# Optimization experiments

Measured on AMD Instinct MI355X. Metric: run time of the kernel, lower is better.

The kernel has to match this reference:

```python
import jax, jax.numpy as jnp
import numpy as np

E, CAP, D, H = 8, 2048, 1024, 4096  # experts, capacity, model_dim, hidden

def setup_inputs() -> dict:
    key = jax.random.key(0)
    k = jax.random.split(key, 5)
    s1 = 1.0 / np.sqrt(D)
    s2 = 1.0 / np.sqrt(H)
    return {
        "x": jax.random.normal(k[0], (E, CAP, D), dtype=jnp.float32),
        "fc1_w": jax.random.uniform(k[1], (E, H, D), jnp.float32, -s1, s1),
        "fc1_b": jax.random.uniform(k[2], (E, H), jnp.float32, -s1, s1),
        "fc2_w": jax.random.uniform(k[3], (E, H, D), jnp.float32, -s2, s2),
        "fc2_b": jax.random.uniform(k[4], (E, D), jnp.float32, -s2, s2),
    }

def reference(x, fc1_w, fc1_b, fc2_w, fc2_b):
    # y = relu(x @ fc1_w^T + b1) @ fc2_w + b2, batched over experts e
    y = jnp.einsum('ecd,ehd->ech', x, fc1_w) + fc1_b[:, None, :]   # [E, CAP, H]
    y = jax.nn.relu(y)
    y = jnp.einsum('ech,ehd->ecd', y, fc2_w) + fc2_b[:, None, :]   # [E, CAP, D]
    return y
```

## Files before the change

kernel.cpp:

```cpp
#include <hip/hip_runtime.h>
#include <hip/hip_bf16.h>
#include <stdint.h>

#define E_    8
#define CAP_  2048
#define D_    1024
#define H_    4096

typedef unsigned short u16;
typedef __attribute__((ext_vector_type(8))) short bf16x8;
typedef __attribute__((ext_vector_type(4))) float f32x4;

__device__ __forceinline__ u16 f2bf(float f) {
    union { float f; unsigned int u; } v; v.f = f;
    unsigned int u = v.u;
    unsigned int r = (u + 0x7fffu + ((u >> 16) & 1u)) >> 16;
    return (u16)r;
}

__device__ __forceinline__ void gload_lds16(const void* g, void* l) {
    __builtin_amdgcn_global_load_lds(
        (const __attribute__((address_space(1))) unsigned int*)g,
        (__attribute__((address_space(3))) unsigned int*)l,
        16, 0, 0);
}

__global__ void cvt_f32_bf16(const float* __restrict__ in, u16* __restrict__ out, int n4) {
    int i = blockIdx.x * blockDim.x + threadIdx.x;
    if (i >= n4) return;
    const float4 v = ((const float4*)in)[i];
    ushort4 o;
    o.x = f2bf(v.x); o.y = f2bf(v.y); o.z = f2bf(v.z); o.w = f2bf(v.w);
    ((ushort4*)out)[i] = o;
}

__global__ void transpose_cvt(const float* __restrict__ in, u16* __restrict__ out) {
    __shared__ float t[64][69];
    const int e  = blockIdx.z;
    const int h0 = blockIdx.y * 64;
    const int d0 = blockIdx.x * 64;
    const float* I = in + (size_t)e * H_ * D_;
    u16* O = out + (size_t)e * D_ * H_;
    const int tid = threadIdx.x;
    const int r  = tid >> 4;
    const int c  = (tid & 15) * 4;
    #pragma unroll
    for (int s = 0; s < 4; ++s) {
        const int h = r + s * 16;
        const float4 v = *(const float4*)&I[(size_t)(h0 + h) * D_ + d0 + c];
        t[h][c] = v.x; t[h][c + 1] = v.y; t[h][c + 2] = v.z; t[h][c + 3] = v.w;
    }
    __syncthreads();
    #pragma unroll
    for (int s = 0; s < 4; ++s) {
        const int d = r + s * 16;
        ushort4 o;
        o.x = f2bf(t[c + 0][d]); o.y = f2bf(t[c + 1][d]);
        o.z = f2bf(t[c + 2][d]); o.w = f2bf(t[c + 3][d]);
        *(ushort4*)&O[(size_t)(d0 + d) * H_ + h0 + c] = o;
    }
}

template<int EPI>
__global__ __launch_bounds__(512, 2) void gemm256(
    const u16* __restrict__ A, const u16* __restrict__ B,
    const float* __restrict__ bias, void* __restrict__ Cv,
    int M, int N, int K, int TM, int TN,
    size_t sA, size_t sB, size_t sBias, size_t sC)
{
    __shared__ __align__(16) u16 lds[2][2][2][128 * 64];

    const int nwg = gridDim.x;
    const int cpx = nwg >> 3;
    const int bid = blockIdx.x;
    const int wg  = (bid & 7) * cpx + (bid >> 3);
    const int tpe = TM * TN;
    const int e   = wg / tpe;
    const int rem = wg - e * tpe;
    const int tn  = rem / TM;
    const int tm  = rem - tn * TM;
    const int row0 = tm << 8;
    const int col0 = tn << 8;

    const u16* Ae = A + (size_t)e * sA;
    const u16* Be = B + (size_t)e * sB;

    const int tid  = threadIdx.x;
    const int lane = tid & 63;
    const int w    = tid >> 6;
    const int wr   = w >> 2;
    const int wc   = w & 3;
    const int wcH  = wc >> 1;
    const int wcL  = wc & 1;
    const int fr   = lane & 15;
    const int fq   = lane >> 4;
    const int cx   = (fq ^ (fr & 7)) << 4;
    const int lo0  = fr * 128 + cx;
    const int lo1  = fr * 128 + (cx ^ 64);
    const int sl   = lane ^ ((lane >> 3) & 7);
    const int NT   = K >> 6;

    const int srow = (w << 4) + (sl >> 3);
    const int scol = (sl & 7) << 3;
    const u16* pA[2][2];
    const u16* pB[2][2];
    #pragma unroll
    for (int l = 0; l < 2; ++l)
        #pragma unroll
        for (int hf = 0; hf < 2; ++hf) {
            pA[l][hf] = Ae + (size_t)(row0 + hf * 128 + srow + l * 8) * K + scol;
            pB[l][hf] = Be + (size_t)(col0 + hf * 128 + srow + l * 8) * K + scol;
        }

    auto stageA = [&](int buf, int hf, bool pred) {
        #pragma unroll
        for (int l = 0; l < 2; ++l) {
            if (pred) gload_lds16(pA[l][hf], &lds[buf][0][hf][(w * 2 + l) * 512]);
            pA[l][hf] += 64;
        }
    };
    auto stageB = [&](int buf, int hf, bool pred) {
        #pragma unroll
        for (int l = 0; l < 2; ++l) {
            if (pred) gload_lds16(pB[l][hf], &lds[buf][1][hf][(w * 2 + l) * 512]);
            pB[l][hf] += 64;
        }
    };

    f32x4 acc[8][4] = {};

    stageB(0, 0, true); stageB(0, 1, true);
    stageA(0, 0, true); stageA(0, 1, true);
    stageB(1, 0, true); stageB(1, 1, true);
    asm volatile("s_waitcnt vmcnt(4)");
    __builtin_amdgcn_s_barrier();

    for (int t = 0; t < NT; ++t) {
        const int db = t & 1;
        const char* Ah = (const char*)&lds[db][0][wr][0];
        const char* Bh = (const char*)&lds[db][1][wcH][0];
        bf16x8 b[4][2];
        #pragma unroll
        for (int n = 0; n < 4; ++n) {
            b[n][0] = *(const bf16x8*)(Bh + wcL * 8192 + n * 2048 + lo0);
            b[n][1] = *(const bf16x8*)(Bh + wcL * 8192 + n * 2048 + lo1);
        }
        #pragma unroll
        for (int p = 0; p < 4; ++p) {
            bf16x8 a[2][2];
            #pragma unroll
            for (int mm = 0; mm < 2; ++mm) {
                a[mm][0] = *(const bf16x8*)(Ah + (2 * p + mm) * 2048 + lo0);
                a[mm][1] = *(const bf16x8*)(Ah + (2 * p + mm) * 2048 + lo1);
            }
            if (p == 0)      stageA(db ^ 1, 0, t + 1 < NT);
            else if (p == 1) stageA(db ^ 1, 1, t + 1 < NT);
            else if (p == 2) stageB(db,     0, t + 2 < NT);
            else             stageB(db,     1, t + 2 < NT);

            __builtin_amdgcn_s_setprio(1);
            #pragma unroll
            for (int kk = 0; kk < 2; ++kk)
                #pragma unroll
                for (int mm = 0; mm < 2; ++mm)
                    #pragma unroll
                    for (int n = 0; n < 4; ++n)
                        acc[2 * p + mm][n] = __builtin_amdgcn_mfma_f32_16x16x32_bf16(
                            a[mm][kk], b[n][kk], acc[2 * p + mm][n], 0, 0, 0);
            __builtin_amdgcn_s_setprio(0);
            if (p == 3) {
                if (t < NT - 2)       asm volatile("s_waitcnt vmcnt(4)");
                else if (t == NT - 2) asm volatile("s_waitcnt vmcnt(0)");
            }
            __builtin_amdgcn_s_barrier();
        }
    }

    const float* be = bias + (size_t)e * sBias;
    if (EPI == 0) {
        u16* cl = (u16*)&lds[0][0][0][0];
        #pragma unroll
        for (int n = 0; n < 4; ++n) {
            const int ccol = wc * 64 + n * 16 + fr;
            const float bv = be[col0 + ccol];
            #pragma unroll
            for (int m = 0; m < 8; ++m) {
                const int crow = wr * 128 + m * 16 + fq * 4;
                #pragma unroll
                for (int i = 0; i < 4; ++i) {
                    float v = acc[m][n][i] + bv;
                    v = v > 0.f ? v : 0.f;
                    cl[(crow + i) * 256 + ccol] = f2bf(v);
                }
            }
        }
        __builtin_amdgcn_s_barrier();
        u16* Ce = (u16*)Cv + (size_t)e * sC;
        const int rr = tid >> 5;
        const int cc = (tid & 31) * 8;
        #pragma unroll
        for (int s = 0; s < 16; ++s) {
            const int row = s * 16 + rr;
            const float4 v = *(const float4*)&cl[row * 256 + cc];
            *(float4*)&Ce[(size_t)(row0 + row) * N + col0 + cc] = v;
        }
    } else {
        float* cf = (float*)&lds[0][0][0][0];
        float* Ce = (float*)Cv + (size_t)e * sC;
        #pragma unroll
        for (int p = 0; p < 2; ++p) {
            __builtin_amdgcn_s_barrier();
            #pragma unroll
            for (int n = 0; n < 4; ++n) {
                const int ccol = wc * 64 + n * 16 + fr;
                const float bv = be[col0 + ccol];
                #pragma unroll
                for (int mm = 0; mm < 4; ++mm) {
                    const int lrow = wr * 64 + mm * 16 + fq * 4;
                    #pragma unroll
                    for (int i = 0; i < 4; ++i)
                        cf[(lrow + i) * 256 + ccol] = acc[p * 4 + mm][n][i] + bv;
                }
            }
            __builtin_amdgcn_s_barrier();
            const int lr = tid >> 6;
            const int cc = (tid & 63) * 4;
            #pragma unroll
            for (int s = 0; s < 16; ++s) {
                const int lrow = s * 8 + lr;
                const int wrr  = lrow >> 6;
                const int rem2 = lrow & 63;
                const int grow = row0 + wrr * 128 + p * 64 + rem2;
                const float4 v = *(const float4*)&cf[lrow * 256 + cc];
                *(float4*)&Ce[(size_t)grow * N + col0 + cc] = v;
            }
        }
    }
}

extern "C" void kernel_launch(void* const* d_in, const int* in_sizes, int n_in,
                              void* d_out, int out_size, void* d_ws, size_t ws_size,
                              hipStream_t stream) {
    (void)in_sizes; (void)n_in; (void)out_size; (void)ws_size;
    const float* x     = (const float*)d_in[0];
    const float* fc1_w = (const float*)d_in[1];
    const float* fc1_b = (const float*)d_in[2];
    const float* fc2_w = (const float*)d_in[3];
    const float* fc2_b = (const float*)d_in[4];
    float* out = (float*)d_out;

    u16* xbf  = (u16*)d_ws;
    u16* w1bf = xbf  + (size_t)E_ * CAP_ * D_;
    u16* w2t  = w1bf + (size_t)E_ * H_ * D_;
    u16* y1   = w2t  + (size_t)E_ * D_ * H_;

    {
        int n4 = E_ * CAP_ * D_ / 4;
        cvt_f32_bf16<<<n4 / 256, 256, 0, stream>>>(x, xbf, n4);
    }
    {
        int n4 = E_ * H_ * D_ / 4;
        cvt_f32_bf16<<<n4 / 256, 256, 0, stream>>>(fc1_w, w1bf, n4);
    }
    transpose_cvt<<<dim3(D_ / 64, H_ / 64, E_), 256, 0, stream>>>(fc2_w, w2t);

    gemm256<0><<<dim3(E_ * (CAP_ / 256) * (H_ / 256)), 512, 0, stream>>>(
        xbf, w1bf, fc1_b, y1, CAP_, H_, D_, CAP_ / 256, H_ / 256,
        (size_t)CAP_ * D_, (size_t)H_ * D_, (size_t)H_, (size_t)CAP_ * H_);

    gemm256<1><<<dim3(E_ * (CAP_ / 256) * (D_ / 256)), 512, 0, stream>>>(
        y1, w2t, fc2_b, out, CAP_, D_, H_, CAP_ / 256, D_ / 256,
        (size_t)CAP_ * H_, (size_t)D_ * H_, (size_t)D_, (size_t)CAP_ * D_);
}
```

Measured before the change: 343.0 us.

## Replace staggered per-phase prefetch with single-stage double buffer and one barrier per tile

Replaces the interleaved A/B prefetch schedule, which issued loads across four phases with per-phase barriers and a two-tiles-ahead B prefetch, with a simple double buffer. All A and B loads for the next tile are issued at the start of each iteration, followed by a full vmcnt(0) wait and one barrier per K-tile. LDS reads of A are software-pipelined against the MFMAs of the previous phase. This removes three barriers per tile, but exposes global load latency because the wait drains all outstanding loads every iteration.

```diff
diff --git a/kernel.cpp b/kernel.cpp
--- a/kernel.cpp
+++ b/kernel.cpp
@@ -112,52 +112,47 @@
             pB[l][hf] = Be + (size_t)(col0 + hf * 128 + srow + l * 8) * K + scol;
         }
 
-    auto stageA = [&](int buf, int hf, bool pred) {
-        #pragma unroll
-        for (int l = 0; l < 2; ++l) {
-            if (pred) gload_lds16(pA[l][hf], &lds[buf][0][hf][(w * 2 + l) * 512]);
-            pA[l][hf] += 64;
-        }
+    auto stage = [&](int buf, bool pred) {
+        #pragma unroll
+        for (int l = 0; l < 2; ++l)
+            #pragma unroll
+            for (int hf = 0; hf < 2; ++hf) {
+                if (pred) {
+                    gload_lds16(pA[l][hf], &lds[buf][0][hf][(w * 2 + l) * 512]);
+                    gload_lds16(pB[l][hf], &lds[buf][1][hf][(w * 2 + l) * 512]);
+                }
+                pA[l][hf] += 64;
+                pB[l][hf] += 64;
+            }
     };
-    auto stageB = [&](int buf, int hf, bool pred) {
-        #pragma unroll
-        for (int l = 0; l < 2; ++l) {
-            if (pred) gload_lds16(pB[l][hf], &lds[buf][1][hf][(w * 2 + l) * 512]);
-            pB[l][hf] += 64;
-        }
-    };
 
     f32x4 acc[8][4] = {};
 
-    stageB(0, 0, true); stageB(0, 1, true);
-    stageA(0, 0, true); stageA(0, 1, true);
-    stageB(1, 0, true); stageB(1, 1, true);
-    asm volatile("s_waitcnt vmcnt(4)");
+    stage(0, true);
+    asm volatile("s_waitcnt vmcnt(0)");
     __builtin_amdgcn_s_barrier();
 
     for (int t = 0; t < NT; ++t) {
         const int db = t & 1;
         const char* Ah = (const char*)&lds[db][0][wr][0];
         const char* Bh = (const char*)&lds[db][1][wcH][0];
+
+        auto rdA = [&](bf16x8 (&a)[2][2], int p) {
+            #pragma unroll
+            for (int mm = 0; mm < 2; ++mm) {
+                a[mm][0] = *(const bf16x8*)(Ah + (2 * p + mm) * 2048 + lo0);
+                a[mm][1] = *(const bf16x8*)(Ah + (2 * p + mm) * 2048 + lo1);
+            }
+        };
+
         bf16x8 b[4][2];
         #pragma unroll
         for (int n = 0; n < 4; ++n) {
             b[n][0] = *(const bf16x8*)(Bh + wcL * 8192 + n * 2048 + lo0);
             b[n][1] = *(const bf16x8*)(Bh + wcL * 8192 + n * 2048 + lo1);
         }
-        #pragma unroll
-        for (int p = 0; p < 4; ++p) {
-            bf16x8 a[2][2];
-            #pragma unroll
-            for (int mm = 0; mm < 2; ++mm) {
-                a[mm][0] = *(const bf16x8*)(Ah + (2 * p + mm) * 2048 + lo0);
-                a[mm][1] = *(const bf16x8*)(Ah + (2 * p + mm) * 2048 + lo1);
-            }
-            if (p == 0)      stageA(db ^ 1, 0, t + 1 < NT);
-            else if (p == 1) stageA(db ^ 1, 1, t + 1 < NT);
-            else if (p == 2) stageB(db,     0, t + 2 < NT);
-            else             stageB(db,     1, t + 2 < NT);
-
+
+        auto domfma = [&](bf16x8 (&a)[2][2], int p) {
             __builtin_amdgcn_s_setprio(1);
             #pragma unroll
             for (int kk = 0; kk < 2; ++kk)
@@ -168,12 +163,18 @@
                         acc[2 * p + mm][n] = __builtin_amdgcn_mfma_f32_16x16x32_bf16(
                             a[mm][kk], b[n][kk], acc[2 * p + mm][n], 0, 0, 0);
             __builtin_amdgcn_s_setprio(0);
-            if (p == 3) {
-                if (t < NT - 2)       asm volatile("s_waitcnt vmcnt(4)");
-                else if (t == NT - 2) asm volatile("s_waitcnt vmcnt(0)");
-            }
-            __builtin_amdgcn_s_barrier();
-        }
+        };
+
+        bf16x8 aA[2][2], aB[2][2];
+        rdA(aA, 0);
+        stage(db ^ 1, t + 1 < NT);
+        rdA(aB, 1); domfma(aA, 0);
+        rdA(aA, 2); domfma(aB, 1);
+        rdA(aB, 3); domfma(aA, 2);
+        domfma(aB, 3);
+
+        asm volatile("s_waitcnt vmcnt(0)");
+        __builtin_amdgcn_s_barrier();
     }
 
     const float* be = bias + (size_t)e * sBias;
```

Result: slower. 366.4 us (+6.8%).

## Restructure GEMM main loop into fenced phases with extra barriers and explicit LDS waits

Applied to the files above, without the earlier changes.

The unrolled k-step loop is rewritten so each of the four sub-phases issues its LDS fragment reads and global-to-LDS prefetch, then hits a workgroup barrier, then waits on lgkmcnt before running the MFMA block. sched_barrier fences pin the instruction order and stop the compiler from interleaving. The aim is a ping-pong style schedule where waves stay in lockstep, so memory issue and matrix-core work alternate cleanly across waves. It doubles the number of s_barrier calls per k-step, which adds synchronisation overhead. The fences also take away the compiler's freedom to overlap LDS reads with MFMAs inside a wave.

```diff
diff --git a/kernel.cpp b/kernel.cpp
--- a/kernel.cpp
+++ b/kernel.cpp
@@ -112,14 +112,14 @@
             pB[l][hf] = Be + (size_t)(col0 + hf * 128 + srow + l * 8) * K + scol;
         }
 
-    auto stageA = [&](int buf, int hf, bool pred) {
+    auto stA = [&](int buf, int hf, bool pred) {
         #pragma unroll
         for (int l = 0; l < 2; ++l) {
             if (pred) gload_lds16(pA[l][hf], &lds[buf][0][hf][(w * 2 + l) * 512]);
             pA[l][hf] += 64;
         }
     };
-    auto stageB = [&](int buf, int hf, bool pred) {
+    auto stB = [&](int buf, int hf, bool pred) {
         #pragma unroll
         for (int l = 0; l < 2; ++l) {
             if (pred) gload_lds16(pB[l][hf], &lds[buf][1][hf][(w * 2 + l) * 512]);
@@ -128,52 +128,88 @@
     };
 
     f32x4 acc[8][4] = {};
-
-    stageB(0, 0, true); stageB(0, 1, true);
-    stageA(0, 0, true); stageA(0, 1, true);
-    stageB(1, 0, true); stageB(1, 1, true);
+    bf16x8 b[4][2], aE[2][2], aO[2][2];
+
+    auto rdA = [&](bf16x8 (&dst)[2][2], const char* Ah, int p) {
+        dst[0][0] = *(const bf16x8*)(Ah + (2 * p + 0) * 2048 + lo0);
+        dst[0][1] = *(const bf16x8*)(Ah + (2 * p + 0) * 2048 + lo1);
+        dst[1][0] = *(const bf16x8*)(Ah + (2 * p + 1) * 2048 + lo0);
+        dst[1][1] = *(const bf16x8*)(Ah + (2 * p + 1) * 2048 + lo1);
+    };
+    auto rdB = [&](const char* Bq) {
+        #pragma unroll
+        for (int n = 0; n < 4; ++n) {
+            b[n][0] = *(const bf16x8*)(Bq + n * 2048 + lo0);
+            b[n][1] = *(const bf16x8*)(Bq + n * 2048 + lo1);
+        }
+    };
+    auto mf = [&](bf16x8 (&a)[2][2], int p) {
+        __builtin_amdgcn_s_setprio(1);
+        #pragma unroll
+        for (int kk = 0; kk < 2; ++kk)
+            #pragma unroll
+            for (int mm = 0; mm < 2; ++mm)
+                #pragma unroll
+                for (int n = 0; n < 4; ++n)
+                    acc[2 * p + mm][n] = __builtin_amdgcn_mfma_f32_16x16x32_bf16(
+                        a[mm][kk], b[n][kk], acc[2 * p + mm][n], 0, 0, 0);
+        __builtin_amdgcn_s_setprio(0);
+    };
+
+    stB(0, 0, true); stB(0, 1, true);
+    stA(0, 0, true); stA(0, 1, true);
+    stB(1, 0, true); stB(1, 1, true);
     asm volatile("s_waitcnt vmcnt(4)");
     __builtin_amdgcn_s_barrier();
 
     for (int t = 0; t < NT; ++t) {
         const int db = t & 1;
         const char* Ah = (const char*)&lds[db][0][wr][0];
-        const char* Bh = (const char*)&lds[db][1][wcH][0];
-        bf16x8 b[4][2];
-        #pragma unroll
-        for (int n = 0; n < 4; ++n) {
-            b[n][0] = *(const bf16x8*)(Bh + wcL * 8192 + n * 2048 + lo0);
-            b[n][1] = *(const bf16x8*)(Bh + wcL * 8192 + n * 2048 + lo1);
-        }
-        #pragma unroll
-        for (int p = 0; p < 4; ++p) {
-            bf16x8 a[2][2];
-            #pragma unroll
-            for (int mm = 0; mm < 2; ++mm) {
-                a[mm][0] = *(const bf16x8*)(Ah + (2 * p + mm) * 2048 + lo0);
-                a[mm][1] = *(const bf16x8*)(Ah + (2 * p + mm) * 2048 + lo1);
-            }
-            if (p == 0)      stageA(db ^ 1, 0, t + 1 < NT);
-            else if (p == 1) stageA(db ^ 1, 1, t + 1 < NT);
-            else if (p == 2) stageB(db,     0, t + 2 < NT);
-            else             stageB(db,     1, t + 2 < NT);
-
-            __builtin_amdgcn_s_setprio(1);
-            #pragma unroll
-            for (int kk = 0; kk < 2; ++kk)
-                #pragma unroll
-                for (int mm = 0; mm < 2; ++mm)
-                    #pragma unroll
-                    for (int n = 0; n < 4; ++n)
-                        acc[2 * p + mm][n] = __builtin_amdgcn_mfma_f32_16x16x32_bf16(
-                            a[mm][kk], b[n][kk], acc[2 * p + mm][n], 0, 0, 0);
-            __builtin_amdgcn_s_setprio(0);
-            if (p == 3) {
-                if (t < NT - 2)       asm volatile("s_waitcnt vmcnt(4)");
-                else if (t == NT - 2) asm volatile("s_waitcnt vmcnt(0)");
-            }
-            __builtin_amdgcn_s_barrier();
-        }
+        const char* Bq = (const char*)&lds[db][1][wcH][0] + wcL * 8192;
+
+        rdB(Bq);
+        rdA(aE, Ah, 0);
+        stA(db ^ 1, 0, t + 1 < NT);
+        __builtin_amdgcn_sched_barrier(0);
+        asm volatile("s_waitcnt lgkmcnt(8)");
+        __builtin_amdgcn_s_barrier();
+        asm volatile("s_waitcnt lgkmcnt(0)");
+        __builtin_amdgcn_sched_barrier(0);
+        mf(aE, 0);
+        __builtin_amdgcn_sched_barrier(0);
+        __builtin_amdgcn_s_barrier();
+
+        rdA(aO, Ah, 1);
+        stA(db ^ 1, 1, t + 1 < NT);
+        __builtin_amdgcn_sched_barrier(0);
+        __builtin_amdgcn_s_barrier();
+        asm volatile("s_waitcnt lgkmcnt(0)");
+        __builtin_amdgcn_sched_barrier(0);
+        mf(aO, 1);
+        __builtin_amdgcn_sched_barrier(0);
+        __builtin_amdgcn_s_barrier();
+
+        rdA(aE, Ah, 2);
+        stB(db, 0, t + 2 < NT);
+        __builtin_amdgcn_sched_barrier(0);
+        __builtin_amdgcn_s_barrier();
+        asm volatile("s_waitcnt lgkmcnt(0)");
+        __builtin_amdgcn_sched_barrier(0);
+        mf(aE, 2);
+        __builtin_amdgcn_sched_barrier(0);
+        __builtin_amdgcn_s_barrier();
+
+        rdA(aO, Ah, 3);
+        stB(db, 1, t + 2 < NT);
+        __builtin_amdgcn_sched_barrier(0);
+        __builtin_amdgcn_s_barrier();
+        asm volatile("s_waitcnt lgkmcnt(0)");
+        __builtin_amdgcn_sched_barrier(0);
+        mf(aO, 3);
+        __builtin_amdgcn_sched_barrier(0);
+        if (t < NT - 2)       asm volatile("s_waitcnt vmcnt(4)");
+        else if (t == NT - 2) asm volatile("s_waitcnt vmcnt(0)");
+        __builtin_amdgcn_s_barrier();
     }
 
     const float* be = bias + (size_t)e * sBias;
```

Measured after the change: 354.1 us. +3.2%, slower.
